# Optimization experiments

Measured on AMD Instinct MI355X. Metric: run time of the kernel, lower is better.

## Reference

```python
import jax, jax.numpy as jnp
import numpy as np

CUTOFF = 5.0           # module init kwarg
NSYS, NAT = 64, 1000   # 64 systems of 1000 atoms each
BOX = 21.544           # cubic box edge -> ~0.1 atoms/A^3 (water-like density)
MAX_PAIRS = 2_200_000


def setup_inputs() -> dict:
    key = jax.random.key(0)
    coords = jax.random.uniform(key, (NSYS * NAT, 3), dtype=jnp.float32) * BOX
    isys = jnp.repeat(jnp.arange(NSYS, dtype=jnp.int32), NAT)
    natoms = jnp.full((NSYS,), NAT, dtype=jnp.int32)
    return {"coordinates": coords, "isys": isys, "natoms": natoms}


def reference(coordinates, isys, natoms):
    # Fixed-capacity cutoff neighbor list (no PBC branch), faithful to
    # GraphGeneratorFixed: half-list (i<j, same system), squared distances d12,
    # compacted into a MAX_PAIRS buffer padded with padding_value=N, then
    # symmetrized by concatenation.
    nsys = natoms.shape[0]
    n = coordinates.shape[0]
    nat = n // nsys                      # equal-sized systems (static)
    padding_value = n
    cutoff2 = jnp.float32(CUTOFF * CUTOFF)

    x = coordinates.reshape(nsys, nat, 3)                 # [S, nat, 3]
    sq = jnp.sum(x * x, axis=-1)                          # [S, nat]
    gram = jnp.einsum('sid,sjd->sij', x, x)               # [S, nat, nat]
    d12 = sq[:, :, None] + sq[:, None, :] - 2.0 * gram    # squared distances

    triu = jnp.triu(jnp.ones((nat, nat), dtype=bool), k=1)  # i < j half-list
    mask = (d12 < cutoff2) & triu[None, :, :]             # [S, nat, nat]
    mflat = mask.reshape(-1)                              # [S*nat*nat]
    npairs = jnp.sum(mflat)

    # stream-compaction: position of each kept pair in the output buffer
    pos = jnp.cumsum(mflat.astype(jnp.int32)) - 1
    sel = jnp.where(mflat, pos, MAX_PAIRS)                # OOB -> dropped
    flat_idx = jnp.arange(nsys * nat * nat, dtype=jnp.int32)
    idx_buf = jnp.full((MAX_PAIRS,), -1, dtype=jnp.int32).at[sel].set(
        flat_idx, mode='drop')

    valid = idx_buf >= 0
    ib = jnp.maximum(idx_buf, 0)
    s = ib // (nat * nat)
    rem = ib % (nat * nat)
    i = rem // nat
    j = rem % nat
    src = jnp.where(valid, s * nat + i, padding_value)
    dst = jnp.where(valid, s * nat + j, padding_value)
    d12_sel = jnp.where(valid, d12.reshape(-1)[ib], cutoff2)

    # symmetrize (directed graph), as in the original
    edge_src = jnp.concatenate([src, dst])
    edge_dst = jnp.concatenate([dst, src])
    d12_out = jnp.concatenate([d12_sel, d12_sel])
    return edge_src, edge_dst, d12_out, npairs
```

## Files before the change

kernel.cpp:

```cpp
#include <hip/hip_runtime.h>

#define NSYS 64
#define NAT  1000
#define NTOT (NSYS * NAT)
#define MP   2200000
#define CUT2 25.0f
#define PADV 64000.0f
#define SCAN_BLOCKS 250
#define CAP  104
#define EB   512
#define LCN  1152
#define NROWS 512
#define POSB  4096

__device__ __forceinline__ float dist2f(float xi, float yi, float zi,
                                        float xj, float yj, float zj) {
    float dx = xi - xj, dy = yi - yj, dz = zi - zj;
    return fmaf(dz, dz, fmaf(dy, dy, dx * dx));
}

__device__ __forceinline__ int mbcnt(unsigned long long m) {
    unsigned lo = __builtin_amdgcn_mbcnt_lo((unsigned)m, 0u);
    return (int)__builtin_amdgcn_mbcnt_hi((unsigned)(m >> 32), lo);
}

__global__ __launch_bounds__(1024) void k_eval(const float* __restrict__ coords,
                                               int* __restrict__ counts,
                                               uint2* __restrict__ qbuf) {
    __shared__ float4 lc[LCN];
    int s      = blockIdx.x >> 3;
    int stripe = blockIdx.x & 7;
    const float* cs = coords + s * (NAT * 3);
    for (int a = threadIdx.x; a < LCN; a += 1024)
        lc[a] = (a < NAT)
              ? make_float4(cs[3 * a], cs[3 * a + 1], cs[3 * a + 2], 0.0f)
              : make_float4(1.0e30f, 1.0e30f, 1.0e30f, 0.0f);
    __syncthreads();
    int w    = threadIdx.x >> 6;
    int lane = threadIdx.x & 63;
    int W    = stripe * 16 + w;
    for (int t = 0;; t++) {
        int r = ((t & 1) ? (127 - W) : W) + (t << 7);
        if (r >= NAT) { if (((t & 1) ? W : (127 - W)) + (t << 7) >= NAT) break; else continue; }
        float4 ci = lc[r];
        int grow = s * NAT + r;
        uint2* q = qbuf + (size_t)grow * CAP;
        int running = 0;
        int jb = r + 1;
        for (; jb + 127 < NAT; jb += 128) {
            int j  = jb + lane;
            float4 c0 = lc[j];
            float4 c1 = lc[j + 64];
            float d0 = dist2f(ci.x, ci.y, ci.z, c0.x, c0.y, c0.z);
            float d1 = dist2f(ci.x, ci.y, ci.z, c1.x, c1.y, c1.z);
            bool k0 = d0 < CUT2;
            bool k1 = d1 < CUT2;
            unsigned long long m0 = __ballot(k0);
            unsigned long long m1 = __ballot(k1);
            if (k0) {
                int rank = running + mbcnt(m0);
                if (rank < CAP)
                    q[rank] = make_uint2((unsigned)(j - r), __float_as_uint(d0));
            }
            int base1 = running + (int)__popcll(m0);
            if (k1) {
                int rank = base1 + mbcnt(m1);
                if (rank < CAP)
                    q[rank] = make_uint2((unsigned)(j + 64 - r), __float_as_uint(d1));
            }
            running = base1 + (int)__popcll(m1);
        }
        if (jb < NAT) {
            int j  = jb + lane;
            int j2 = j + 64;
            float4 c0 = lc[j];
            float4 c1 = lc[j2];
            float d0 = dist2f(ci.x, ci.y, ci.z, c0.x, c0.y, c0.z);
            float d1 = dist2f(ci.x, ci.y, ci.z, c1.x, c1.y, c1.z);
            bool k0 = (j  < NAT) && (d0 < CUT2);
            bool k1 = (j2 < NAT) && (d1 < CUT2);
            unsigned long long m0 = __ballot(k0);
            unsigned long long m1 = __ballot(k1);
            if (k0) {
                int rank = running + mbcnt(m0);
                if (rank < CAP)
                    q[rank] = make_uint2((unsigned)(j - r), __float_as_uint(d0));
            }
            int base1 = running + (int)__popcll(m0);
            if (k1) {
                int rank = base1 + mbcnt(m1);
                if (rank < CAP)
                    q[rank] = make_uint2((unsigned)(j2 - r), __float_as_uint(d1));
            }
            running = base1 + (int)__popcll(m1);
        }
        if (lane == 0) counts[grow] = running;
    }
}

__global__ void k_scan_a(const int* __restrict__ counts, int* __restrict__ offs,
                         int* __restrict__ bsum) {
    __shared__ int tmp[256];
    int t = threadIdx.x;
    int g = blockIdx.x * 256 + t;
    int v = counts[g];
    tmp[t] = v;
    __syncthreads();
    for (int off = 1; off < 256; off <<= 1) {
        int u = (t >= off) ? tmp[t - off] : 0;
        __syncthreads();
        tmp[t] += u;
        __syncthreads();
    }
    offs[g] = tmp[t] - v;
    if (t == 255) bsum[blockIdx.x] = tmp[255];
}

__global__ __launch_bounds__(1024) void k_emit(const int* __restrict__ offs,
                                               const int* __restrict__ bsum,
                                               const uint2* __restrict__ qbuf,
                                               float* __restrict__ out) {
    __shared__ int bpre[256];
    __shared__ int lgoff[NROWS + 1];
    __shared__ int sh_r0, sh_tot;
    int t = threadIdx.x;
    int v = 0;
    if (t < 256) {
        v = (t < SCAN_BLOCKS) ? bsum[t] : 0;
        bpre[t] = v;
    }
    __syncthreads();
    for (int off = 1; off < 256; off <<= 1) {
        int u = 0;
        if (t < 256 && t >= off) u = bpre[t - off];
        __syncthreads();
        if (t < 256) bpre[t] += u;
        __syncthreads();
    }
    int incl = (t < 256) ? bpre[t] : 0;
    __syncthreads();
    if (t < 256) bpre[t] = incl - v;
    if (t == 255) sh_tot = incl;
    __syncthreads();
    int total = sh_tot;

    int p0 = blockIdx.x * POSB;
    if (t == 0) {
        int lo = 0, hi = NTOT;
        while (lo < hi) {
            int mid = (lo + hi + 1) >> 1;
            int g = (mid < NTOT) ? offs[mid] + bpre[mid >> 8] : total;
            if (g <= p0) lo = mid; else hi = mid - 1;
        }
        sh_r0 = lo;
    }
    __syncthreads();
    int r0 = sh_r0;
    if (t <= NROWS) {
        int r = r0 + t;
        lgoff[t] = (r < NTOT) ? offs[r] + bpre[r >> 8] : total;
    }
    __syncthreads();

    if (blockIdx.x == 0 && t == 0) out[6 * MP] = (float)total;
    int valid = total < MP ? total : MP;

    int p4 = p0 + t * 4;
    if (p4 >= MP) return;
    int k = 0;
    for (int step = 256; step; step >>= 1) {
        int nk = k + step;
        if (nk <= NROWS - 1 && lgoff[nk] <= p4) k = nk;
    }
    float fs[4], fd[4], dd[4];
#pragma unroll
    for (int e = 0; e < 4; e++) {
        int p = p4 + e;
        if (p < valid) {
            while (k < NROWS - 1 && lgoff[k + 1] <= p) k++;
            int row = r0 + k;
            int local = p - lgoff[k];
            if (local > CAP - 1) local = CAP - 1;
            uint2 rec = qbuf[(size_t)row * CAP + local];
            fs[e] = (float)row;
            fd[e] = (float)(row + (int)rec.x);
            dd[e] = __uint_as_float(rec.y);
        } else {
            fs[e] = PADV; fd[e] = PADV; dd[e] = CUT2;
        }
    }
    if (p4 + 4 <= MP) {
        float4 vs = {fs[0], fs[1], fs[2], fs[3]};
        float4 vd = {fd[0], fd[1], fd[2], fd[3]};
        float4 vv = {dd[0], dd[1], dd[2], dd[3]};
        *(float4*)(out + p4)          = vs;
        *(float4*)(out + MP + p4)     = vd;
        *(float4*)(out + 2 * MP + p4) = vd;
        *(float4*)(out + 3 * MP + p4) = vs;
        *(float4*)(out + 4 * MP + p4) = vv;
        *(float4*)(out + 5 * MP + p4) = vv;
    } else {
#pragma unroll
        for (int e = 0; e < 4; e++) {
            int p = p4 + e;
            if (p < MP) {
                out[p]          = fs[e];
                out[MP + p]     = fd[e];
                out[2 * MP + p] = fd[e];
                out[3 * MP + p] = fs[e];
                out[4 * MP + p] = dd[e];
                out[5 * MP + p] = dd[e];
            }
        }
    }
}

extern "C" void kernel_launch(void* const* d_in, const int* in_sizes, int n_in,
                              void* d_out, int out_size, void* d_ws, size_t ws_size,
                              hipStream_t stream) {
    const float* coords = (const float*)d_in[0];
    float* out = (float*)d_out;

    int*   counts = (int*)d_ws;
    int*   offs   = counts + NTOT;
    int*   bsum   = offs + NTOT;
    uint2* qbuf   = (uint2*)(bsum + 256);

    int emit_blocks = (MP + POSB - 1) / POSB;
    k_eval<<<EB, 1024, 0, stream>>>(coords, counts, qbuf);
    k_scan_a<<<SCAN_BLOCKS, 256, 0, stream>>>(counts, offs, bsum);
    k_emit<<<emit_blocks, 1024, 0, stream>>>(offs, bsum, qbuf, out);
}
```

Baseline: 113.1 us.

## Fold scan kernel into eval atomics and per-block local scans in emit

```diff
diff --git a/kernel.cpp b/kernel.cpp
--- a/kernel.cpp
+++ b/kernel.cpp
@@ -6,7 +6,7 @@
 #define MP   2200000
 #define CUT2 25.0f
 #define PADV 64000.0f
-#define SCAN_BLOCKS 250
+#define NBLK 250
 #define CAP  104
 #define EB   512
 #define LCN  1152
@@ -26,6 +26,7 @@
 
 __global__ __launch_bounds__(1024) void k_eval(const float* __restrict__ coords,
                                                int* __restrict__ counts,
+                                               int* __restrict__ bsum,
                                                uint2* __restrict__ qbuf) {
     __shared__ float4 lc[LCN];
     int s      = blockIdx.x >> 3;
@@ -94,39 +95,26 @@
             }
             running = base1 + (int)__popcll(m1);
         }
-        if (lane == 0) counts[grow] = running;
-    }
-}
-
-__global__ void k_scan_a(const int* __restrict__ counts, int* __restrict__ offs,
-                         int* __restrict__ bsum) {
-    __shared__ int tmp[256];
-    int t = threadIdx.x;
-    int g = blockIdx.x * 256 + t;
-    int v = counts[g];
-    tmp[t] = v;
-    __syncthreads();
-    for (int off = 1; off < 256; off <<= 1) {
-        int u = (t >= off) ? tmp[t - off] : 0;
-        __syncthreads();
-        tmp[t] += u;
-        __syncthreads();
-    }
-    offs[g] = tmp[t] - v;
-    if (t == 255) bsum[blockIdx.x] = tmp[255];
-}
-
-__global__ __launch_bounds__(1024) void k_emit(const int* __restrict__ offs,
+        if (lane == 0) {
+            counts[grow] = running;
+            atomicAdd(&bsum[grow >> 8], running);
+        }
+    }
+}
+
+__global__ __launch_bounds__(1024) void k_emit(const int* __restrict__ counts,
                                                const int* __restrict__ bsum,
                                                const uint2* __restrict__ qbuf,
                                                float* __restrict__ out) {
     __shared__ int bpre[256];
+    __shared__ int scnt[768];
     __shared__ int lgoff[NROWS + 1];
-    __shared__ int sh_r0, sh_tot;
+    __shared__ int sh_b0, sh_r0, sh_tot;
     int t = threadIdx.x;
+
     int v = 0;
     if (t < 256) {
-        v = (t < SCAN_BLOCKS) ? bsum[t] : 0;
+        v = (t < NBLK) ? bsum[t] : 0;
         bpre[t] = v;
     }
     __syncthreads();
@@ -143,22 +131,51 @@
     if (t == 255) sh_tot = incl;
     __syncthreads();
     int total = sh_tot;
-
     int p0 = blockIdx.x * POSB;
-    if (t == 0) {
-        int lo = 0, hi = NTOT;
-        while (lo < hi) {
-            int mid = (lo + hi + 1) >> 1;
-            int g = (mid < NTOT) ? offs[mid] + bpre[mid >> 8] : total;
-            if (g <= p0) lo = mid; else hi = mid - 1;
-        }
-        sh_r0 = lo;
+
+    if (t == 0) sh_b0 = 0;
+    __syncthreads();
+    if (t < NBLK && bpre[t] <= p0) atomicMax(&sh_b0, t);
+    __syncthreads();
+    int b0 = sh_b0;
+
+    int cv = 0;
+    if (t < 768) {
+        int g = b0 * 256 + t;
+        cv = (g < NTOT) ? counts[g] : 0;
+        scnt[t] = cv;
+    }
+    __syncthreads();
+    for (int off = 1; off < 256; off <<= 1) {
+        int u = 0;
+        if (t < 768 && (t & 255) >= off) u = scnt[t - off];
+        __syncthreads();
+        if (t < 768) scnt[t] += u;
+        __syncthreads();
+    }
+    int cincl = (t < 768) ? scnt[t] : 0;
+    __syncthreads();
+    if (t < 768) scnt[t] = cincl - cv;
+    __syncthreads();
+
+    if (t == 0) sh_r0 = (p0 < total) ? b0 * 256 : NTOT;
+    __syncthreads();
+    if (p0 < total && t < 256) {
+        int g = b0 * 256 + t;
+        if (g < NTOT && bpre[b0] + scnt[t] <= p0) atomicMax(&sh_r0, g);
     }
     __syncthreads();
     int r0 = sh_r0;
+
     if (t <= NROWS) {
         int r = r0 + t;
-        lgoff[t] = (r < NTOT) ? offs[r] + bpre[r >> 8] : total;
+        int lg;
+        if (r >= NTOT) lg = total;
+        else {
+            int blk = r >> 8;
+            lg = bpre[blk] + scnt[(blk - b0) * 256 + (r & 255)];
+        }
+        lgoff[t] = lg;
     }
     __syncthreads();
 
@@ -222,12 +239,11 @@
     float* out = (float*)d_out;
 
     int*   counts = (int*)d_ws;
-    int*   offs   = counts + NTOT;
-    int*   bsum   = offs + NTOT;
+    int*   bsum   = counts + NTOT;
     uint2* qbuf   = (uint2*)(bsum + 256);
 
+    hipMemsetAsync(bsum, 0, NBLK * sizeof(int), stream);
+    k_eval<<<EB, 1024, 0, stream>>>(coords, counts, bsum, qbuf);
     int emit_blocks = (MP + POSB - 1) / POSB;
-    k_eval<<<EB, 1024, 0, stream>>>(coords, counts, qbuf);
-    k_scan_a<<<SCAN_BLOCKS, 256, 0, stream>>>(counts, offs, bsum);
-    k_emit<<<emit_blocks, 1024, 0, stream>>>(offs, bsum, qbuf, out);
-}
+    k_emit<<<emit_blocks, 1024, 0, stream>>>(counts, bsum, qbuf, out);
+}
```

Result: slower. 205.8 us (+81.9%).
